# Kernel optimization log

Measured on AMD Instinct MI355X. Metric: run time of the kernel, lower is better.

## Reference

```python
import jax, jax.numpy as jnp
import numpy as np

C, N, E = 5, 50000, 800000   # relations (categories), nodes per category, edges per relation
DIN, H, DOUT = 128, 128, 64


def setup_inputs() -> dict:
    key = jax.random.key(0)
    ks = jax.random.split(key, 7)
    x = jax.random.normal(ks[0], (C, N, DIN), dtype=jnp.float32)
    edge_index = jax.random.randint(ks[1], (C, 2, E), 0, N)
    edge_weight = jax.random.uniform(ks[2], (C, E), dtype=jnp.float32, minval=0.1, maxval=1.0)
    W1 = jax.random.normal(ks[3], (C, DIN, H), dtype=jnp.float32) * (1.0 / np.sqrt(DIN))
    b1 = jnp.zeros((C, H), dtype=jnp.float32)
    W2 = jax.random.normal(ks[4], (C, H, DOUT), dtype=jnp.float32) * (1.0 / np.sqrt(H))
    b2 = jnp.zeros((C, DOUT), dtype=jnp.float32)
    return {"x": x, "edge_index": edge_index, "edge_weight": edge_weight,
            "W1": W1, "b1": b1, "W2": W2, "b2": b2}


def gcn_layer(x, src, dst, w, W, b):
    """PyG GCNConv: linear -> symmetric-normalized weighted scatter-add -> bias.
    Self-loops added with weight 1 (PyG default add_self_loops=True)."""
    n = x.shape[0]
    loop = jnp.arange(n)
    s = jnp.concatenate([src, loop])          # [E+N]
    d = jnp.concatenate([dst, loop])
    wa = jnp.concatenate([w, jnp.ones((n,), w.dtype)])
    deg = jax.ops.segment_sum(wa, d, num_segments=n)      # weighted in-degree (col)
    deg_safe = jnp.where(deg > 0, deg, 1.0)
    dis = jnp.where(deg > 0, jax.lax.rsqrt(deg_safe), 0.0)  # deg^-1/2, inf->0
    norm = dis[s] * wa * dis[d]                # [E+N]
    h = x @ W                                  # [N, F_out] transform before propagation
    msg = norm[:, None] * h[s]                 # gather + scale
    out = jnp.zeros((n, W.shape[1]), x.dtype).at[d].add(msg)  # scatter-add
    return out + b


def reference(x, edge_index, edge_weight, W1, b1, W2, b2):
    def per_relation(xc, ei, ew, w1, bb1, w2, bb2):
        h = jax.nn.relu(gcn_layer(xc, ei[0], ei[1], ew, w1, bb1))
        return gcn_layer(h, ei[0], ei[1], ew, w2, bb2)
    # Each node type receives from exactly one relation, so HeteroConv's 'sum'
    # aggregation is the identity; vmap over the 5 independent relations.
    return jax.vmap(per_relation)(x, edge_index, edge_weight, W1, b1, W2, b2)
```

## Files before the change

kernel.cpp:

```cpp
#include <hip/hip_runtime.h>
#include <hip/hip_fp16.h>

#define C_REL 5
#define NN    50000
#define EE    800000
#define D_IN  128
#define D_H   128
#define D_OUT 64

static constexpr int CN = C_REL * NN;
static constexpr int CE = C_REL * EE;
static constexpr int SCAN_B = (NN + 255) / 256;
static constexpr int BLK_GEMM_REL = (NN + 63) / 64;
static constexpr int BLK_AGG_REL  = NN / 4;
static constexpr int GEMM_BLOCKS  = C_REL * BLK_GEMM_REL;
static constexpr int HIST_BLOCKS  = 4096;
static constexpr int FUSED_GRID   = 2 * HIST_BLOCKS;
static constexpr int FILL_BLOCKS  = 4096;

static constexpr unsigned long long MASK40 = (1ULL << 40) - 1;
static constexpr float FIX_SCALE = 16777216.0f;
static constexpr float FIX_INV   = 1.0f / 16777216.0f;

__device__ inline unsigned pack2h(float a, float b) {
  __half2 h = __floats2half2_rn(a, b);
  return *reinterpret_cast<unsigned*>(&h);
}


__global__ __launch_bounds__(256) void init_kernel(unsigned long long* packed) {
  int i = blockIdx.x * 256 + threadIdx.x;
  if (i < CN) packed[i] = 0ULL;
}

__device__ inline void hist_body(int bid, int nblocks,
                                 const int* __restrict__ ei,
                                 const float* __restrict__ ew,
                                 unsigned long long* packed,
                                 int* __restrict__ pos) {
  int stride = nblocks * 256;
  for (int idx = bid * 256 + threadIdx.x; idx < CE; idx += stride) {
    int c = idx / EE, e = idx - c * EE;
    int d = ei[(c * 2 + 1) * EE + e];
    float w = ew[idx];
    unsigned long long wfix = (unsigned long long)(w * FIX_SCALE + 0.5f);
    unsigned long long old = atomicAdd(&packed[c * NN + d], (1ULL << 40) | wfix);
    pos[idx] = (int)(old >> 40);
  }
}

__global__ __launch_bounds__(256) void dis_kernel(const unsigned long long* __restrict__ packed,
                                                  float* __restrict__ dis) {
  int i = blockIdx.x * 256 + threadIdx.x;
  if (i >= CN) return;
  float deg = 1.0f + (float)(packed[i] & MASK40) * FIX_INV;
  dis[i] = rsqrtf(deg);
}

__global__ __launch_bounds__(256) void scan_a_kernel(const unsigned long long* __restrict__ packed,
                                                     int* rowptr, int* bsum) {
  int c = blockIdx.x / SCAN_B;
  int b = blockIdx.x - c * SCAN_B;
  int tid = threadIdx.x;
  int i = b * 256 + tid;
  int val = (i < NN) ? (int)(packed[c * NN + i] >> 40) : 0;
  __shared__ int sh[256];
  sh[tid] = val;
  __syncthreads();
  for (int off = 1; off < 256; off <<= 1) {
    int t = (tid >= off) ? sh[tid - off] : 0;
    __syncthreads();
    sh[tid] += t;
    __syncthreads();
  }
  if (i < NN) rowptr[c * (NN + 1) + i + 1] = sh[tid];
  if (tid == 255) bsum[c * 256 + b] = sh[255];
}

__global__ __launch_bounds__(256) void scan_b_kernel(int* bsum) {
  int c = blockIdx.x;
  int tid = threadIdx.x;
  int val = (tid < SCAN_B) ? bsum[c * 256 + tid] : 0;
  __shared__ int sh[256];
  sh[tid] = val;
  __syncthreads();
  for (int off = 1; off < 256; off <<= 1) {
    int t = (tid >= off) ? sh[tid - off] : 0;
    __syncthreads();
    sh[tid] += t;
    __syncthreads();
  }
  bsum[c * 256 + tid] = sh[tid] - val;
}

__global__ __launch_bounds__(256) void scan_c_kernel(int* rowptr, const int* __restrict__ bsum) {
  int c = blockIdx.x / SCAN_B;
  int b = blockIdx.x - c * SCAN_B;
  int i = b * 256 + threadIdx.x;
  if (i < NN) rowptr[c * (NN + 1) + i + 1] += bsum[c * 256 + b];
  if (i == 0) rowptr[c * (NN + 1)] = 0;
}

__global__ __launch_bounds__(256) void fill_kernel(const int* __restrict__ ei,
                                                   const float* __restrict__ ew,
                                                   const float* __restrict__ dis,
                                                   const int* __restrict__ rowptr,
                                                   const int* __restrict__ pos,
                                                   unsigned* __restrict__ csr) {
  int stride = gridDim.x * 256;
  for (int idx = blockIdx.x * 256 + threadIdx.x; idx < CE; idx += stride) {
    int c = idx / EE, e = idx - c * EE;
    int s = ei[(c * 2 + 0) * EE + e];
    int d = ei[(c * 2 + 1) * EE + e];
    float w = ew[idx];
    float nrm = dis[c * NN + s] * w * dis[c * NN + d];
    int slot = rowptr[c * (NN + 1) + d] + pos[idx];
    unsigned ent = (unsigned)s | ((unsigned)__half_as_ushort(__float2half_rn(nrm)) << 16);
    csr[(size_t)c * EE + slot] = ent;
  }
}


template <int NC, bool AHALF>
__device__ inline void gemm_body(int bid, const void* __restrict__ Av,
                                 const float* __restrict__ B,
                                 __half* __restrict__ Cout) {
  constexpr int K = 128;
  constexpr int KC = 32;
  constexpr int CPT = NC / 32;
  __shared__ float Bs[KC * NC];
  __shared__ float As[64][KC + 4];

  int c  = bid / BLK_GEMM_REL;
  int bl = bid - c * BLK_GEMM_REL;
  const float* Bc = B + (size_t)c * K * NC;
  __half* Cc = Cout + (size_t)c * NN * NC;

  int tid = threadIdx.x;
  int tx = tid & 31;
  int ty = tid >> 5;
  int rowBase = bl * 64;

  float acc[8][CPT];
#pragma unroll
  for (int i = 0; i < 8; ++i)
#pragma unroll
    for (int j = 0; j < CPT; ++j) acc[i][j] = 0.f;

  for (int kc = 0; kc < K; kc += KC) {
    __syncthreads();
    {
      const float4* B4 = (const float4*)(Bc + (size_t)kc * NC);
      float4* Bs4 = (float4*)Bs;
#pragma unroll
      for (int i = tid; i < KC * NC / 4; i += 256) Bs4[i] = B4[i];
    }
    if constexpr (AHALF) {
      const __half* Ac = (const __half*)Av + (size_t)c * NN * K;
      int lr = tid >> 2;
      int lc = (tid & 3) * 8;
      int gr = rowBase + lr;
      uint4 v = make_uint4(0u, 0u, 0u, 0u);
      if (gr < NN) v = *(const uint4*)&Ac[(size_t)gr * K + kc + lc];
      const __half2* hp = (const __half2*)&v;
#pragma unroll
      for (int j = 0; j < 4; ++j) {
        float2 f = __half22float2(hp[j]);
        As[lr][lc + 2 * j]     = f.x;
        As[lr][lc + 2 * j + 1] = f.y;
      }
    } else {
      const float* Ac = (const float*)Av + (size_t)c * NN * K;
      int lr = tid >> 3;
      int lc = (tid & 7) * 4;
#pragma unroll
      for (int rr = 0; rr < 64; rr += 32) {
        int r = lr + rr;
        int gr = rowBase + r;
        float4 v = make_float4(0.f, 0.f, 0.f, 0.f);
        if (gr < NN) v = *(const float4*)&Ac[(size_t)gr * K + kc + lc];
        *(float4*)&As[r][lc] = v;
      }
    }
    __syncthreads();

#pragma unroll
    for (int kk = 0; kk < KC; kk += 4) {
      float4 av[8];
#pragma unroll
      for (int i = 0; i < 8; ++i) av[i] = *(const float4*)&As[ty * 8 + i][kk];
#pragma unroll
      for (int u = 0; u < 4; ++u) {
        int k = kk + u;
        if constexpr (CPT == 4) {
          float4 bv = *(const float4*)&Bs[k * NC + tx * 4];
#pragma unroll
          for (int i = 0; i < 8; ++i) {
            float a = ((const float*)&av[i])[u];
            acc[i][0] += a * bv.x;
            acc[i][1] += a * bv.y;
            acc[i][2] += a * bv.z;
            acc[i][3] += a * bv.w;
          }
        } else {
          float2 bv = *(const float2*)&Bs[k * NC + tx * 2];
#pragma unroll
          for (int i = 0; i < 8; ++i) {
            float a = ((const float*)&av[i])[u];
            acc[i][0] += a * bv.x;
            acc[i][1] += a * bv.y;
          }
        }
      }
    }
  }

#pragma unroll
  for (int i = 0; i < 8; ++i) {
    int gr = rowBase + ty * 8 + i;
    if (gr >= NN) continue;
    if constexpr (CPT == 4) {
      unsigned lo = pack2h(acc[i][0], acc[i][1]);
      unsigned hi = pack2h(acc[i][2], acc[i][3]);
      *(uint2*)&Cc[(size_t)gr * NC + tx * 4] = make_uint2(lo, hi);
    } else {
      *(unsigned*)&Cc[(size_t)gr * NC + tx * 2] = pack2h(acc[i][0], acc[i][1]);
    }
  }
}

__global__ __launch_bounds__(256) void fused_hist_gemm1_kernel(
    const float* __restrict__ x, const float* __restrict__ W1, __half* __restrict__ h1,
    const int* __restrict__ ei, const float* __restrict__ ew,
    unsigned long long* packed, int* __restrict__ pos) {
  int id = blockIdx.x;
  if (id & 1) {
    hist_body(id >> 1, HIST_BLOCKS, ei, ew, packed, pos);
  } else {
    int gid = id >> 1;
    if (gid < GEMM_BLOCKS) gemm_body<D_H, false>(gid, x, W1, h1);
  }
}

__global__ __launch_bounds__(256) void gemm2_kernel(const __half* __restrict__ A,
                                                    const float* __restrict__ B,
                                                    __half* __restrict__ Cout) {
  gemm_body<D_OUT, true>(blockIdx.x, A, B, Cout);
}


__global__ __launch_bounds__(256) void agg1_kernel(const __half2* __restrict__ h,
                                                   const int* __restrict__ rowptr,
                                                   const unsigned* __restrict__ csr,
                                                   const float* __restrict__ dis,
                                                   const float* __restrict__ bias,
                                                   __half* __restrict__ out) {
  int c  = blockIdx.x / BLK_AGG_REL;
  int bl = blockIdx.x - c * BLK_AGG_REL;
  int node = bl * 4 + (threadIdx.x >> 6);
  int lane = threadIdx.x & 63;

  const __half2* hc = h + (size_t)c * NN * 64;
  const unsigned* csrc = csr + (size_t)c * EE;
  int beg = rowptr[c * (NN + 1) + node];
  int end = rowptr[c * (NN + 1) + node + 1];

  float a0 = 0.f, a1 = 0.f;
  int idx = beg;
  for (; idx + 4 <= end; idx += 4) {
    unsigned e0 = csrc[idx], e1 = csrc[idx + 1], e2 = csrc[idx + 2], e3 = csrc[idx + 3];
    float2 v0 = __half22float2(hc[(size_t)(e0 & 0xffffu) * 64 + lane]);
    float2 v1 = __half22float2(hc[(size_t)(e1 & 0xffffu) * 64 + lane]);
    float2 v2 = __half22float2(hc[(size_t)(e2 & 0xffffu) * 64 + lane]);
    float2 v3 = __half22float2(hc[(size_t)(e3 & 0xffffu) * 64 + lane]);
    float n0 = __half2float(__ushort_as_half((unsigned short)(e0 >> 16)));
    float n1 = __half2float(__ushort_as_half((unsigned short)(e1 >> 16)));
    float n2 = __half2float(__ushort_as_half((unsigned short)(e2 >> 16)));
    float n3 = __half2float(__ushort_as_half((unsigned short)(e3 >> 16)));
    a0 += n0 * v0.x + n1 * v1.x + n2 * v2.x + n3 * v3.x;
    a1 += n0 * v0.y + n1 * v1.y + n2 * v2.y + n3 * v3.y;
  }
  for (; idx < end; ++idx) {
    unsigned e = csrc[idx];
    float2 v = __half22float2(hc[(size_t)(e & 0xffffu) * 64 + lane]);
    float nm = __half2float(__ushort_as_half((unsigned short)(e >> 16)));
    a0 += nm * v.x;
    a1 += nm * v.y;
  }
  float dn = dis[c * NN + node];
  float sn = dn * dn;
  float2 hv = __half22float2(hc[(size_t)node * 64 + lane]);
  int f = lane * 2;
  a0 += sn * hv.x + bias[c * 128 + f];
  a1 += sn * hv.y + bias[c * 128 + f + 1];
  a0 = fmaxf(a0, 0.f);
  a1 = fmaxf(a1, 0.f);
  ((unsigned*)out)[((size_t)c * NN + node) * 64 + lane] = pack2h(a0, a1);
}


__global__ __launch_bounds__(256) void agg2_kernel(const __half2* __restrict__ h,
                                                   const int* __restrict__ rowptr,
                                                   const unsigned* __restrict__ csr,
                                                   const float* __restrict__ dis,
                                                   const float* __restrict__ bias,
                                                   float* __restrict__ out) {
  int c  = blockIdx.x / BLK_AGG_REL;
  int bl = blockIdx.x - c * BLK_AGG_REL;
  int node = bl * 4 + (threadIdx.x >> 6);
  int lane = threadIdx.x & 63;
  int hf = lane >> 5;
  int fl = lane & 31;

  const __half2* hc = h + (size_t)c * NN * 32;
  const unsigned* csrc = csr + (size_t)c * EE;
  int beg = rowptr[c * (NN + 1) + node];
  int end = rowptr[c * (NN + 1) + node + 1];

  float a0 = 0.f, a1 = 0.f;
  int idx = beg + hf;
  for (; idx + 2 < end; idx += 4) {
    unsigned ea = csrc[idx], eb = csrc[idx + 2];
    float2 va = __half22float2(hc[(size_t)(ea & 0xffffu) * 32 + fl]);
    float2 vb = __half22float2(hc[(size_t)(eb & 0xffffu) * 32 + fl]);
    float na = __half2float(__ushort_as_half((unsigned short)(ea >> 16)));
    float nb = __half2float(__ushort_as_half((unsigned short)(eb >> 16)));
    a0 += na * va.x + nb * vb.x;
    a1 += na * va.y + nb * vb.y;
  }
  for (; idx < end; idx += 2) {
    unsigned e = csrc[idx];
    float2 v = __half22float2(hc[(size_t)(e & 0xffffu) * 32 + fl]);
    float nm = __half2float(__ushort_as_half((unsigned short)(e >> 16)));
    a0 += nm * v.x;
    a1 += nm * v.y;
  }
  a0 += __shfl_xor(a0, 32, 64);
  a1 += __shfl_xor(a1, 32, 64);
  if (hf == 0) {
    float dn = dis[c * NN + node];
    float sn = dn * dn;
    float2 hv = __half22float2(hc[(size_t)node * 32 + fl]);
    int f = fl * 2;
    a0 += sn * hv.x + bias[c * 64 + f];
    a1 += sn * hv.y + bias[c * 64 + f + 1];
    *(float2*)&out[((size_t)c * NN + node) * 64 + f] = make_float2(a0, a1);
  }
}


extern "C" void kernel_launch(void* const* d_in, const int* in_sizes, int n_in,
                              void* d_out, int out_size, void* d_ws, size_t ws_size,
                              hipStream_t stream) {
  const float* x  = (const float*)d_in[0];
  const int*   ei = (const int*)d_in[1];
  const float* ew = (const float*)d_in[2];
  const float* W1 = (const float*)d_in[3];
  const float* b1 = (const float*)d_in[4];
  const float* W2 = (const float*)d_in[5];
  const float* b2 = (const float*)d_in[6];
  float* out = (float*)d_out;

  char* ws = (char*)d_ws;
  size_t off = 0;
  auto alloc = [&](size_t bytes) {
    size_t cur = off;
    off += (bytes + 255) & ~(size_t)255;
    return cur;
  };
  unsigned long long* packed = (unsigned long long*)(ws + alloc((size_t)CN * 8));
  float*    dis    = (float*)   (ws + alloc((size_t)CN * 4));
  int*      rowptr = (int*)     (ws + alloc((size_t)C_REL * (NN + 1) * 4));
  int*      bsum   = (int*)     (ws + alloc((size_t)C_REL * 256 * 4));
  unsigned* csr    = (unsigned*)(ws + alloc((size_t)CE * 4));
  __half*   h1     = (__half*)  (ws + alloc((size_t)CN * D_H * 2));
  __half*   agg1h  = (__half*)  (ws + alloc((size_t)CN * D_H * 2));
  int* pos = (int*)agg1h;

  const int NB_CN = (CN + 255) / 256;

  init_kernel<<<NB_CN, 256, 0, stream>>>(packed);
  fused_hist_gemm1_kernel<<<FUSED_GRID, 256, 0, stream>>>(x, W1, h1, ei, ew, packed, pos);
  dis_kernel<<<NB_CN, 256, 0, stream>>>(packed, dis);
  scan_a_kernel<<<C_REL * SCAN_B, 256, 0, stream>>>(packed, rowptr, bsum);
  scan_b_kernel<<<C_REL, 256, 0, stream>>>(bsum);
  scan_c_kernel<<<C_REL * SCAN_B, 256, 0, stream>>>(rowptr, bsum);
  fill_kernel<<<FILL_BLOCKS, 256, 0, stream>>>(ei, ew, dis, rowptr, pos, csr);

  agg1_kernel<<<C_REL * BLK_AGG_REL, 256, 0, stream>>>((const __half2*)h1, rowptr, csr,
                                                       dis, b1, agg1h);
  gemm2_kernel<<<C_REL * BLK_GEMM_REL, 256, 0, stream>>>(agg1h, W2, h1);
  agg2_kernel<<<C_REL * BLK_AGG_REL, 256, 0, stream>>>((const __half2*)h1, rowptr, csr,
                                                       dis, b2, out);
}
```

Baseline: 726.3 us.

## Split feature matrices into 32-wide column chunks for cache-friendly gather aggregation

The GEMMs now write h1 and h2 in a chunked layout of 32 halfs (64 bytes) per node per chunk, and gemm2 reads agg1h in the same layout. The aggregation kernels launch one block set per chunk, and each wave processes four edges at a time with 16-lane groups, combining them with shuffles. Each pass gathers from a smaller working set that is more likely to stay in L2/MALL, but the CSR is re-read once per chunk. Separately, the dis computation is folded into scan_a so the dis_kernel launch is removed.

```diff
diff --git a/kernel.cpp b/kernel.cpp
--- a/kernel.cpp
+++ b/kernel.cpp
@@ -49,21 +49,19 @@
   }
 }
 
-__global__ __launch_bounds__(256) void dis_kernel(const unsigned long long* __restrict__ packed,
-                                                  float* __restrict__ dis) {
-  int i = blockIdx.x * 256 + threadIdx.x;
-  if (i >= CN) return;
-  float deg = 1.0f + (float)(packed[i] & MASK40) * FIX_INV;
-  dis[i] = rsqrtf(deg);
-}
-
 __global__ __launch_bounds__(256) void scan_a_kernel(const unsigned long long* __restrict__ packed,
-                                                     int* rowptr, int* bsum) {
+                                                     int* rowptr, int* bsum,
+                                                     float* __restrict__ dis) {
   int c = blockIdx.x / SCAN_B;
   int b = blockIdx.x - c * SCAN_B;
   int tid = threadIdx.x;
   int i = b * 256 + tid;
-  int val = (i < NN) ? (int)(packed[c * NN + i] >> 40) : 0;
+  int val = 0;
+  if (i < NN) {
+    unsigned long long p = packed[c * NN + i];
+    val = (int)(p >> 40);
+    dis[c * NN + i] = rsqrtf(1.0f + (float)(p & MASK40) * FIX_INV);
+  }
   __shared__ int sh[256];
   sh[tid] = val;
   __syncthreads();
@@ -134,7 +132,6 @@
   int c  = bid / BLK_GEMM_REL;
   int bl = bid - c * BLK_GEMM_REL;
   const float* Bc = B + (size_t)c * K * NC;
-  __half* Cc = Cout + (size_t)c * NN * NC;
 
   int tid = threadIdx.x;
   int tx = tid & 31;
@@ -156,12 +153,12 @@
       for (int i = tid; i < KC * NC / 4; i += 256) Bs4[i] = B4[i];
     }
     if constexpr (AHALF) {
-      const __half* Ac = (const __half*)Av + (size_t)c * NN * K;
+      const __half* Ac = (const __half*)Av + ((size_t)(c * 4 + (kc >> 5))) * NN * 32;
       int lr = tid >> 2;
       int lc = (tid & 3) * 8;
       int gr = rowBase + lr;
       uint4 v = make_uint4(0u, 0u, 0u, 0u);
-      if (gr < NN) v = *(const uint4*)&Ac[(size_t)gr * K + kc + lc];
+      if (gr < NN) v = *(const uint4*)&Ac[(size_t)gr * 32 + lc];
       const __half2* hp = (const __half2*)&v;
 #pragma unroll
       for (int j = 0; j < 4; ++j) {
@@ -220,11 +217,13 @@
     int gr = rowBase + ty * 8 + i;
     if (gr >= NN) continue;
     if constexpr (CPT == 4) {
+      __half* Cc = Cout + ((size_t)(c * 4 + (tx >> 3))) * NN * 32;
       unsigned lo = pack2h(acc[i][0], acc[i][1]);
       unsigned hi = pack2h(acc[i][2], acc[i][3]);
-      *(uint2*)&Cc[(size_t)gr * NC + tx * 4] = make_uint2(lo, hi);
+      *(uint2*)&Cc[(size_t)gr * 32 + (tx & 7) * 4] = make_uint2(lo, hi);
     } else {
-      *(unsigned*)&Cc[(size_t)gr * NC + tx * 2] = pack2h(acc[i][0], acc[i][1]);
+      __half* Cc = Cout + ((size_t)(c * 2 + (tx >> 4))) * NN * 32;
+      *(unsigned*)&Cc[(size_t)gr * 32 + (tx & 15) * 2] = pack2h(acc[i][0], acc[i][1]);
     }
   }
 }
@@ -255,49 +254,55 @@
                                                    const float* __restrict__ dis,
                                                    const float* __restrict__ bias,
                                                    __half* __restrict__ out) {
-  int c  = blockIdx.x / BLK_AGG_REL;
-  int bl = blockIdx.x - c * BLK_AGG_REL;
+  int id = blockIdx.x;
+  int cp = id / BLK_AGG_REL;
+  int bl = id - cp * BLK_AGG_REL;
+  int c = cp >> 2, chunk = cp & 3;
   int node = bl * 4 + (threadIdx.x >> 6);
   int lane = threadIdx.x & 63;
-
-  const __half2* hc = h + (size_t)c * NN * 64;
+  int eg = lane >> 4;
+  int fl = lane & 15;
+
+  const __half2* hc = h + ((size_t)(c * 4 + chunk)) * NN * 16;
   const unsigned* csrc = csr + (size_t)c * EE;
   int beg = rowptr[c * (NN + 1) + node];
   int end = rowptr[c * (NN + 1) + node + 1];
 
   float a0 = 0.f, a1 = 0.f;
-  int idx = beg;
-  for (; idx + 4 <= end; idx += 4) {
-    unsigned e0 = csrc[idx], e1 = csrc[idx + 1], e2 = csrc[idx + 2], e3 = csrc[idx + 3];
-    float2 v0 = __half22float2(hc[(size_t)(e0 & 0xffffu) * 64 + lane]);
-    float2 v1 = __half22float2(hc[(size_t)(e1 & 0xffffu) * 64 + lane]);
-    float2 v2 = __half22float2(hc[(size_t)(e2 & 0xffffu) * 64 + lane]);
-    float2 v3 = __half22float2(hc[(size_t)(e3 & 0xffffu) * 64 + lane]);
-    float n0 = __half2float(__ushort_as_half((unsigned short)(e0 >> 16)));
-    float n1 = __half2float(__ushort_as_half((unsigned short)(e1 >> 16)));
-    float n2 = __half2float(__ushort_as_half((unsigned short)(e2 >> 16)));
-    float n3 = __half2float(__ushort_as_half((unsigned short)(e3 >> 16)));
-    a0 += n0 * v0.x + n1 * v1.x + n2 * v2.x + n3 * v3.x;
-    a1 += n0 * v0.y + n1 * v1.y + n2 * v2.y + n3 * v3.y;
-  }
-  for (; idx < end; ++idx) {
+  int idx = beg + eg;
+  for (; idx + 4 < end; idx += 8) {
+    unsigned ea = csrc[idx], eb = csrc[idx + 4];
+    float2 va = __half22float2(hc[(size_t)(ea & 0xffffu) * 16 + fl]);
+    float2 vb = __half22float2(hc[(size_t)(eb & 0xffffu) * 16 + fl]);
+    float na = __half2float(__ushort_as_half((unsigned short)(ea >> 16)));
+    float nb = __half2float(__ushort_as_half((unsigned short)(eb >> 16)));
+    a0 += na * va.x + nb * vb.x;
+    a1 += na * va.y + nb * vb.y;
+  }
+  for (; idx < end; idx += 4) {
     unsigned e = csrc[idx];
-    float2 v = __half22float2(hc[(size_t)(e & 0xffffu) * 64 + lane]);
+    float2 v = __half22float2(hc[(size_t)(e & 0xffffu) * 16 + fl]);
     float nm = __half2float(__ushort_as_half((unsigned short)(e >> 16)));
     a0 += nm * v.x;
     a1 += nm * v.y;
   }
-  float dn = dis[c * NN + node];
-  float sn = dn * dn;
-  float2 hv = __half22float2(hc[(size_t)node * 64 + lane]);
-  int f = lane * 2;
-  a0 += sn * hv.x + bias[c * 128 + f];
-  a1 += sn * hv.y + bias[c * 128 + f + 1];
-  a0 = fmaxf(a0, 0.f);
-  a1 = fmaxf(a1, 0.f);
-  ((unsigned*)out)[((size_t)c * NN + node) * 64 + lane] = pack2h(a0, a1);
-}
-
+  a0 += __shfl_xor(a0, 16, 64);
+  a1 += __shfl_xor(a1, 16, 64);
+  a0 += __shfl_xor(a0, 32, 64);
+  a1 += __shfl_xor(a1, 32, 64);
+  if (lane < 16) {
+    float dn = dis[c * NN + node];
+    float sn = dn * dn;
+    float2 hv = __half22float2(hc[(size_t)node * 16 + fl]);
+    int f = chunk * 32 + fl * 2;
+    a0 += sn * hv.x + bias[c * 128 + f];
+    a1 += sn * hv.y + bias[c * 128 + f + 1];
+    a0 = fmaxf(a0, 0.f);
+    a1 = fmaxf(a1, 0.f);
+    ((unsigned*)out)[((size_t)(c * 4 + chunk)) * NN * 16 + (size_t)node * 16 + fl] =
+        pack2h(a0, a1);
+  }
+}
 
 __global__ __launch_bounds__(256) void agg2_kernel(const __half2* __restrict__ h,
                                                    const int* __restrict__ rowptr,
@@ -305,43 +310,47 @@
                                                    const float* __restrict__ dis,
                                                    const float* __restrict__ bias,
                                                    float* __restrict__ out) {
-  int c  = blockIdx.x / BLK_AGG_REL;
-  int bl = blockIdx.x - c * BLK_AGG_REL;
+  int id = blockIdx.x;
+  int cp = id / BLK_AGG_REL;
+  int bl = id - cp * BLK_AGG_REL;
+  int c = cp >> 1, chunk = cp & 1;
   int node = bl * 4 + (threadIdx.x >> 6);
   int lane = threadIdx.x & 63;
-  int hf = lane >> 5;
-  int fl = lane & 31;
-
-  const __half2* hc = h + (size_t)c * NN * 32;
+  int eg = lane >> 4;
+  int fl = lane & 15;
+
+  const __half2* hc = h + ((size_t)(c * 2 + chunk)) * NN * 16;
   const unsigned* csrc = csr + (size_t)c * EE;
   int beg = rowptr[c * (NN + 1) + node];
   int end = rowptr[c * (NN + 1) + node + 1];
 
   float a0 = 0.f, a1 = 0.f;
-  int idx = beg + hf;
-  for (; idx + 2 < end; idx += 4) {
-    unsigned ea = csrc[idx], eb = csrc[idx + 2];
-    float2 va = __half22float2(hc[(size_t)(ea & 0xffffu) * 32 + fl]);
-    float2 vb = __half22float2(hc[(size_t)(eb & 0xffffu) * 32 + fl]);
+  int idx = beg + eg;
+  for (; idx + 4 < end; idx += 8) {
+    unsigned ea = csrc[idx], eb = csrc[idx + 4];
+    float2 va = __half22float2(hc[(size_t)(ea & 0xffffu) * 16 + fl]);
+    float2 vb = __half22float2(hc[(size_t)(eb & 0xffffu) * 16 + fl]);
     float na = __half2float(__ushort_as_half((unsigned short)(ea >> 16)));
     float nb = __half2float(__ushort_as_half((unsigned short)(eb >> 16)));
     a0 += na * va.x + nb * vb.x;
     a1 += na * va.y + nb * vb.y;
   }
-  for (; idx < end; idx += 2) {
+  for (; idx < end; idx += 4) {
     unsigned e = csrc[idx];
-    float2 v = __half22float2(hc[(size_t)(e & 0xffffu) * 32 + fl]);
+    float2 v = __half22float2(hc[(size_t)(e & 0xffffu) * 16 + fl]);
     float nm = __half2float(__ushort_as_half((unsigned short)(e >> 16)));
     a0 += nm * v.x;
     a1 += nm * v.y;
   }
+  a0 += __shfl_xor(a0, 16, 64);
+  a1 += __shfl_xor(a1, 16, 64);
   a0 += __shfl_xor(a0, 32, 64);
   a1 += __shfl_xor(a1, 32, 64);
-  if (hf == 0) {
+  if (lane < 16) {
     float dn = dis[c * NN + node];
     float sn = dn * dn;
-    float2 hv = __half22float2(hc[(size_t)node * 32 + fl]);
-    int f = fl * 2;
+    float2 hv = __half22float2(hc[(size_t)node * 16 + fl]);
+    int f = chunk * 32 + fl * 2;
     a0 += sn * hv.x + bias[c * 64 + f];
     a1 += sn * hv.y + bias[c * 64 + f + 1];
     *(float2*)&out[((size_t)c * NN + node) * 64 + f] = make_float2(a0, a1);
@@ -381,15 +390,14 @@
 
   init_kernel<<<NB_CN, 256, 0, stream>>>(packed);
   fused_hist_gemm1_kernel<<<FUSED_GRID, 256, 0, stream>>>(x, W1, h1, ei, ew, packed, pos);
-  dis_kernel<<<NB_CN, 256, 0, stream>>>(packed, dis);
-  scan_a_kernel<<<C_REL * SCAN_B, 256, 0, stream>>>(packed, rowptr, bsum);
+  scan_a_kernel<<<C_REL * SCAN_B, 256, 0, stream>>>(packed, rowptr, bsum, dis);
   scan_b_kernel<<<C_REL, 256, 0, stream>>>(bsum);
   scan_c_kernel<<<C_REL * SCAN_B, 256, 0, stream>>>(rowptr, bsum);
   fill_kernel<<<FILL_BLOCKS, 256, 0, stream>>>(ei, ew, dis, rowptr, pos, csr);
 
-  agg1_kernel<<<C_REL * BLK_AGG_REL, 256, 0, stream>>>((const __half2*)h1, rowptr, csr,
-                                                       dis, b1, agg1h);
+  agg1_kernel<<<C_REL * 4 * BLK_AGG_REL, 256, 0, stream>>>((const __half2*)h1, rowptr,
+                                                           csr, dis, b1, agg1h);
   gemm2_kernel<<<C_REL * BLK_GEMM_REL, 256, 0, stream>>>(agg1h, W2, h1);
-  agg2_kernel<<<C_REL * BLK_AGG_REL, 256, 0, stream>>>((const __half2*)h1, rowptr, csr,
-                                                       dis, b2, out);
-}
+  agg2_kernel<<<C_REL * 2 * BLK_AGG_REL, 256, 0, stream>>>((const __half2*)h1, rowptr,
+                                                           csr, dis, b2, out);
+}
```

Result: slower. 975.0 us (+34.2%).

## Pack degree histogram into 32-bit atomics and overlap CSR fill with per-relation agg1

Applied to the files above, without the earlier changes.

Shrinks the packed count/weight histogram from 64-bit to 32-bit atomics (10-bit count, 22-bit fixed-point weight sum). Folds the dis computation into scan_a and replaces the scan_b pass with a per-block warp reduction in scan_c. The CSR fill is split per relation, and the fill for relation c+1 is interleaved into the agg1 launch for relation c, so the scatter-heavy fill overlaps with the gather-heavy aggregation. agg1 now reads edges as uint4 after an alignment prologue, uses readfirstlane for the row bounds and 32-bit indexing, and pos moves into the output buffer. The 16-bit fractional weight and 10-bit count limit precision and cap in-degree at 1023, which holds only for these random graphs.

```diff
diff --git a/kernel.cpp b/kernel.cpp
--- a/kernel.cpp
+++ b/kernel.cpp
@@ -16,11 +16,12 @@
 static constexpr int GEMM_BLOCKS  = C_REL * BLK_GEMM_REL;
 static constexpr int HIST_BLOCKS  = 4096;
 static constexpr int FUSED_GRID   = 2 * HIST_BLOCKS;
-static constexpr int FILL_BLOCKS  = 4096;
-
-static constexpr unsigned long long MASK40 = (1ULL << 40) - 1;
-static constexpr float FIX_SCALE = 16777216.0f;
-static constexpr float FIX_INV   = 1.0f / 16777216.0f;
+static constexpr int FILL0_BLOCKS = 1024;
+static constexpr int AGGF_GRID    = 13750;
+static constexpr int FILLS_BLOCKS = 1250;
+
+static constexpr float FIX16     = 65536.0f;
+static constexpr float FIX16_INV = 1.0f / 65536.0f;
 
 __device__ inline unsigned pack2h(float a, float b) {
   __half2 h = __floats2half2_rn(a, b);
@@ -28,42 +29,40 @@
 }
 
 
-__global__ __launch_bounds__(256) void init_kernel(unsigned long long* packed) {
+__global__ __launch_bounds__(256) void init_kernel(unsigned* packed) {
   int i = blockIdx.x * 256 + threadIdx.x;
-  if (i < CN) packed[i] = 0ULL;
+  if (i < CN) packed[i] = 0u;
 }
 
 __device__ inline void hist_body(int bid, int nblocks,
                                  const int* __restrict__ ei,
                                  const float* __restrict__ ew,
-                                 unsigned long long* packed,
+                                 unsigned* packed,
                                  int* __restrict__ pos) {
   int stride = nblocks * 256;
   for (int idx = bid * 256 + threadIdx.x; idx < CE; idx += stride) {
     int c = idx / EE, e = idx - c * EE;
     int d = ei[(c * 2 + 1) * EE + e];
     float w = ew[idx];
-    unsigned long long wfix = (unsigned long long)(w * FIX_SCALE + 0.5f);
-    unsigned long long old = atomicAdd(&packed[c * NN + d], (1ULL << 40) | wfix);
-    pos[idx] = (int)(old >> 40);
-  }
-}
-
-__global__ __launch_bounds__(256) void dis_kernel(const unsigned long long* __restrict__ packed,
-                                                  float* __restrict__ dis) {
-  int i = blockIdx.x * 256 + threadIdx.x;
-  if (i >= CN) return;
-  float deg = 1.0f + (float)(packed[i] & MASK40) * FIX_INV;
-  dis[i] = rsqrtf(deg);
-}
-
-__global__ __launch_bounds__(256) void scan_a_kernel(const unsigned long long* __restrict__ packed,
-                                                     int* rowptr, int* bsum) {
+    unsigned wfix = (unsigned)(w * FIX16 + 0.5f);
+    unsigned old = atomicAdd(&packed[c * NN + d], wfix | (1u << 22));
+    pos[idx] = (int)(old >> 22);
+  }
+}
+
+__global__ __launch_bounds__(256) void scan_a_kernel(const unsigned* __restrict__ packed,
+                                                     int* rowptr, int* bsum,
+                                                     float* __restrict__ dis) {
   int c = blockIdx.x / SCAN_B;
   int b = blockIdx.x - c * SCAN_B;
   int tid = threadIdx.x;
   int i = b * 256 + tid;
-  int val = (i < NN) ? (int)(packed[c * NN + i] >> 40) : 0;
+  int val = 0;
+  if (i < NN) {
+    unsigned p = packed[c * NN + i];
+    val = (int)(p >> 22);
+    dis[c * NN + i] = rsqrtf(1.0f + (float)(p & 0x3FFFFFu) * FIX16_INV);
+  }
   __shared__ int sh[256];
   sh[tid] = val;
   __syncthreads();
@@ -77,47 +76,51 @@
   if (tid == 255) bsum[c * 256 + b] = sh[255];
 }
 
-__global__ __launch_bounds__(256) void scan_b_kernel(int* bsum) {
-  int c = blockIdx.x;
-  int tid = threadIdx.x;
-  int val = (tid < SCAN_B) ? bsum[c * 256 + tid] : 0;
-  __shared__ int sh[256];
-  sh[tid] = val;
-  __syncthreads();
-  for (int off = 1; off < 256; off <<= 1) {
-    int t = (tid >= off) ? sh[tid - off] : 0;
-    __syncthreads();
-    sh[tid] += t;
-    __syncthreads();
-  }
-  bsum[c * 256 + tid] = sh[tid] - val;
-}
-
 __global__ __launch_bounds__(256) void scan_c_kernel(int* rowptr, const int* __restrict__ bsum) {
   int c = blockIdx.x / SCAN_B;
   int b = blockIdx.x - c * SCAN_B;
-  int i = b * 256 + threadIdx.x;
-  if (i < NN) rowptr[c * (NN + 1) + i + 1] += bsum[c * 256 + b];
+  int tid = threadIdx.x;
+  int lane = tid & 63;
+  int acc = 0;
+  for (int t = lane; t < b; t += 64) acc += bsum[c * 256 + t];
+#pragma unroll
+  for (int o = 1; o < 64; o <<= 1) acc += __shfl_xor(acc, o, 64);
+  int i = b * 256 + tid;
+  if (i < NN) rowptr[c * (NN + 1) + i + 1] += acc;
   if (i == 0) rowptr[c * (NN + 1)] = 0;
 }
 
-__global__ __launch_bounds__(256) void fill_kernel(const int* __restrict__ ei,
-                                                   const float* __restrict__ ew,
-                                                   const float* __restrict__ dis,
-                                                   const int* __restrict__ rowptr,
-                                                   const int* __restrict__ pos,
-                                                   unsigned* __restrict__ csr) {
-  int stride = gridDim.x * 256;
-  for (int idx = blockIdx.x * 256 + threadIdx.x; idx < CE; idx += stride) {
-    int c = idx / EE, e = idx - c * EE;
-    int s = ei[(c * 2 + 0) * EE + e];
-    int d = ei[(c * 2 + 1) * EE + e];
-    float w = ew[idx];
-    float nrm = dis[c * NN + s] * w * dis[c * NN + d];
-    int slot = rowptr[c * (NN + 1) + d] + pos[idx];
+__device__ inline void fill_rel_body(int c, int bid, int nblocks,
+                                     const int* __restrict__ ei,
+                                     const float* __restrict__ ew,
+                                     const float* __restrict__ dis,
+                                     const int* __restrict__ rowptr,
+                                     const int* __restrict__ pos,
+                                     unsigned* __restrict__ csr) {
+  int stride = nblocks * 256;
+  const int* srcp = ei + (size_t)(c * 2) * EE;
+  const int* dstp = srcp + EE;
+  const float* ewc = ew + (size_t)c * EE;
+  const int* posc = pos + (size_t)c * EE;
+  const float* disc = dis + c * NN;
+  const int* rpc = rowptr + c * (NN + 1);
+  unsigned* csrc = csr + (size_t)c * EE;
+  for (int e = bid * 256 + threadIdx.x; e < EE; e += stride) {
+    int s = srcp[e];
+    int d = dstp[e];
+    float nrm = disc[s] * ewc[e] * disc[d];
     unsigned ent = (unsigned)s | ((unsigned)__half_as_ushort(__float2half_rn(nrm)) << 16);
-    csr[(size_t)c * EE + slot] = ent;
-  }
+    csrc[rpc[d] + posc[e]] = ent;
+  }
+}
+
+__global__ __launch_bounds__(256) void fill0_kernel(const int* __restrict__ ei,
+                                                    const float* __restrict__ ew,
+                                                    const float* __restrict__ dis,
+                                                    const int* __restrict__ rowptr,
+                                                    const int* __restrict__ pos,
+                                                    unsigned* __restrict__ csr) {
+  fill_rel_body(0, blockIdx.x, FILL0_BLOCKS, ei, ew, dis, rowptr, pos, csr);
 }
 
 
@@ -232,7 +235,7 @@
 __global__ __launch_bounds__(256) void fused_hist_gemm1_kernel(
     const float* __restrict__ x, const float* __restrict__ W1, __half* __restrict__ h1,
     const int* __restrict__ ei, const float* __restrict__ ew,
-    unsigned long long* packed, int* __restrict__ pos) {
+    unsigned* packed, int* __restrict__ pos) {
   int id = blockIdx.x;
   if (id & 1) {
     hist_body(id >> 1, HIST_BLOCKS, ei, ew, packed, pos);
@@ -249,53 +252,71 @@
 }
 
 
-__global__ __launch_bounds__(256) void agg1_kernel(const __half2* __restrict__ h,
-                                                   const int* __restrict__ rowptr,
-                                                   const unsigned* __restrict__ csr,
-                                                   const float* __restrict__ dis,
-                                                   const float* __restrict__ bias,
-                                                   __half* __restrict__ out) {
-  int c  = blockIdx.x / BLK_AGG_REL;
-  int bl = blockIdx.x - c * BLK_AGG_REL;
+__device__ inline void agg1_body(int bid, const __half2* __restrict__ h,
+                                 const int* __restrict__ rowptr,
+                                 const unsigned* __restrict__ csr,
+                                 const float* __restrict__ dis,
+                                 const float* __restrict__ bias,
+                                 __half* __restrict__ out) {
+  int c  = bid / BLK_AGG_REL;
+  int bl = bid - c * BLK_AGG_REL;
   int node = bl * 4 + (threadIdx.x >> 6);
   int lane = threadIdx.x & 63;
 
-  const __half2* hc = h + (size_t)c * NN * 64;
+  const __half2* hc = h + (size_t)c * (NN * 64);
   const unsigned* csrc = csr + (size_t)c * EE;
-  int beg = rowptr[c * (NN + 1) + node];
-  int end = rowptr[c * (NN + 1) + node + 1];
+  int beg = __builtin_amdgcn_readfirstlane(rowptr[c * (NN + 1) + node]);
+  int end = __builtin_amdgcn_readfirstlane(rowptr[c * (NN + 1) + node + 1]);
 
   float a0 = 0.f, a1 = 0.f;
+#define AGG1_EDGE(ent)                                             \
+  {                                                                \
+    unsigned _e = (ent);                                           \
+    unsigned _off = (_e & 0xffffu) * 64u + (unsigned)lane;         \
+    float2 _v = __half22float2(hc[_off]);                          \
+    float _nm = __half2float(__ushort_as_half((unsigned short)(_e >> 16))); \
+    a0 += _nm * _v.x;                                              \
+    a1 += _nm * _v.y;                                              \
+  }
   int idx = beg;
+  int hd = min(end, (beg + 3) & ~3);
+  for (; idx < hd; ++idx) AGG1_EDGE(csrc[idx]);
   for (; idx + 4 <= end; idx += 4) {
-    unsigned e0 = csrc[idx], e1 = csrc[idx + 1], e2 = csrc[idx + 2], e3 = csrc[idx + 3];
-    float2 v0 = __half22float2(hc[(size_t)(e0 & 0xffffu) * 64 + lane]);
-    float2 v1 = __half22float2(hc[(size_t)(e1 & 0xffffu) * 64 + lane]);
-    float2 v2 = __half22float2(hc[(size_t)(e2 & 0xffffu) * 64 + lane]);
-    float2 v3 = __half22float2(hc[(size_t)(e3 & 0xffffu) * 64 + lane]);
-    float n0 = __half2float(__ushort_as_half((unsigned short)(e0 >> 16)));
-    float n1 = __half2float(__ushort_as_half((unsigned short)(e1 >> 16)));
-    float n2 = __half2float(__ushort_as_half((unsigned short)(e2 >> 16)));
-    float n3 = __half2float(__ushort_as_half((unsigned short)(e3 >> 16)));
-    a0 += n0 * v0.x + n1 * v1.x + n2 * v2.x + n3 * v3.x;
-    a1 += n0 * v0.y + n1 * v1.y + n2 * v2.y + n3 * v3.y;
-  }
-  for (; idx < end; ++idx) {
-    unsigned e = csrc[idx];
-    float2 v = __half22float2(hc[(size_t)(e & 0xffffu) * 64 + lane]);
-    float nm = __half2float(__ushort_as_half((unsigned short)(e >> 16)));
-    a0 += nm * v.x;
-    a1 += nm * v.y;
-  }
+    uint4 q = *(const uint4*)(csrc + idx);
+    AGG1_EDGE(q.x);
+    AGG1_EDGE(q.y);
+    AGG1_EDGE(q.z);
+    AGG1_EDGE(q.w);
+  }
+  for (; idx < end; ++idx) AGG1_EDGE(csrc[idx]);
+#undef AGG1_EDGE
+
   float dn = dis[c * NN + node];
   float sn = dn * dn;
-  float2 hv = __half22float2(hc[(size_t)node * 64 + lane]);
+  float2 hv = __half22float2(hc[(unsigned)node * 64u + (unsigned)lane]);
   int f = lane * 2;
   a0 += sn * hv.x + bias[c * 128 + f];
   a1 += sn * hv.y + bias[c * 128 + f + 1];
   a0 = fmaxf(a0, 0.f);
   a1 = fmaxf(a1, 0.f);
   ((unsigned*)out)[((size_t)c * NN + node) * 64 + lane] = pack2h(a0, a1);
+}
+
+__global__ __launch_bounds__(256) void fused_agg1_fill_kernel(
+    int c, const __half2* __restrict__ h, const int* __restrict__ rowptr,
+    const unsigned* __restrict__ csr, const float* __restrict__ dis,
+    const float* __restrict__ bias, __half* __restrict__ out,
+    const int* __restrict__ ei, const float* __restrict__ ew,
+    const int* __restrict__ pos) {
+  int i = blockIdx.x;
+  int r = i % 11;
+  if (r < 10) {
+    int aid = (i / 11) * 10 + r;
+    agg1_body(c * BLK_AGG_REL + aid, h, rowptr, csr, dis, bias, out);
+  } else if (c + 1 < C_REL) {
+    fill_rel_body(c + 1, i / 11, FILLS_BLOCKS, ei, ew, dis, rowptr, pos,
+                  (unsigned*)csr);
+  }
 }
 
 
@@ -312,17 +333,17 @@
   int hf = lane >> 5;
   int fl = lane & 31;
 
-  const __half2* hc = h + (size_t)c * NN * 32;
+  const __half2* hc = h + (size_t)c * (NN * 32);
   const unsigned* csrc = csr + (size_t)c * EE;
-  int beg = rowptr[c * (NN + 1) + node];
-  int end = rowptr[c * (NN + 1) + node + 1];
+  int beg = __builtin_amdgcn_readfirstlane(rowptr[c * (NN + 1) + node]);
+  int end = __builtin_amdgcn_readfirstlane(rowptr[c * (NN + 1) + node + 1]);
 
   float a0 = 0.f, a1 = 0.f;
   int idx = beg + hf;
   for (; idx + 2 < end; idx += 4) {
     unsigned ea = csrc[idx], eb = csrc[idx + 2];
-    float2 va = __half22float2(hc[(size_t)(ea & 0xffffu) * 32 + fl]);
-    float2 vb = __half22float2(hc[(size_t)(eb & 0xffffu) * 32 + fl]);
+    float2 va = __half22float2(hc[(ea & 0xffffu) * 32u + (unsigned)fl]);
+    float2 vb = __half22float2(hc[(eb & 0xffffu) * 32u + (unsigned)fl]);
     float na = __half2float(__ushort_as_half((unsigned short)(ea >> 16)));
     float nb = __half2float(__ushort_as_half((unsigned short)(eb >> 16)));
     a0 += na * va.x + nb * vb.x;
@@ -330,7 +351,7 @@
   }
   for (; idx < end; idx += 2) {
     unsigned e = csrc[idx];
-    float2 v = __half22float2(hc[(size_t)(e & 0xffffu) * 32 + fl]);
+    float2 v = __half22float2(hc[(e & 0xffffu) * 32u + (unsigned)fl]);
     float nm = __half2float(__ushort_as_half((unsigned short)(e >> 16)));
     a0 += nm * v.x;
     a1 += nm * v.y;
@@ -340,7 +361,7 @@
   if (hf == 0) {
     float dn = dis[c * NN + node];
     float sn = dn * dn;
-    float2 hv = __half22float2(hc[(size_t)node * 32 + fl]);
+    float2 hv = __half22float2(hc[(unsigned)node * 32u + (unsigned)fl]);
     int f = fl * 2;
     a0 += sn * hv.x + bias[c * 64 + f];
     a1 += sn * hv.y + bias[c * 64 + f + 1];
@@ -368,28 +389,28 @@
     off += (bytes + 255) & ~(size_t)255;
     return cur;
   };
-  unsigned long long* packed = (unsigned long long*)(ws + alloc((size_t)CN * 8));
+  unsigned* packed = (unsigned*)(ws + alloc((size_t)CN * 4));
   float*    dis    = (float*)   (ws + alloc((size_t)CN * 4));
   int*      rowptr = (int*)     (ws + alloc((size_t)C_REL * (NN + 1) * 4));
   int*      bsum   = (int*)     (ws + alloc((size_t)C_REL * 256 * 4));
   unsigned* csr    = (unsigned*)(ws + alloc((size_t)CE * 4));
   __half*   h1     = (__half*)  (ws + alloc((size_t)CN * D_H * 2));
   __half*   agg1h  = (__half*)  (ws + alloc((size_t)CN * D_H * 2));
-  int* pos = (int*)agg1h;
+  int* pos = (int*)out;
 
   const int NB_CN = (CN + 255) / 256;
 
   init_kernel<<<NB_CN, 256, 0, stream>>>(packed);
   fused_hist_gemm1_kernel<<<FUSED_GRID, 256, 0, stream>>>(x, W1, h1, ei, ew, packed, pos);
-  dis_kernel<<<NB_CN, 256, 0, stream>>>(packed, dis);
-  scan_a_kernel<<<C_REL * SCAN_B, 256, 0, stream>>>(packed, rowptr, bsum);
-  scan_b_kernel<<<C_REL, 256, 0, stream>>>(bsum);
+  scan_a_kernel<<<C_REL * SCAN_B, 256, 0, stream>>>(packed, rowptr, bsum, dis);
   scan_c_kernel<<<C_REL * SCAN_B, 256, 0, stream>>>(rowptr, bsum);
-  fill_kernel<<<FILL_BLOCKS, 256, 0, stream>>>(ei, ew, dis, rowptr, pos, csr);
-
-  agg1_kernel<<<C_REL * BLK_AGG_REL, 256, 0, stream>>>((const __half2*)h1, rowptr, csr,
-                                                       dis, b1, agg1h);
+  fill0_kernel<<<FILL0_BLOCKS, 256, 0, stream>>>(ei, ew, dis, rowptr, pos, csr);
+
+  for (int c = 0; c < C_REL; ++c) {
+    fused_agg1_fill_kernel<<<AGGF_GRID, 256, 0, stream>>>(
+        c, (const __half2*)h1, rowptr, csr, dis, b1, agg1h, ei, ew, pos);
+  }
   gemm2_kernel<<<C_REL * BLK_GEMM_REL, 256, 0, stream>>>(agg1h, W2, h1);
-  agg2_kernel<<<C_REL * BLK_AGG_REL, 256, 0, stream>>>((const __half2*)h1, rowptr, csr,
-                                                       dis, b2, out);
-}
+  agg2_kernel<<<C_REL * BLK_AGG_REL, 256, 0, stream>>>((const __half2*)h1, rowptr,
+                                                       csr, dis, b2, out);
+}
```

Result: no change. 714.8 us, median of 2 (-1.6%).
